# Kernel tuning notes

Measured on AMD Instinct MI355X. Metric: run time of the kernel, lower is better.

Reference implementation:

```python
import jax, jax.numpy as jnp
import numpy as np

L, B, D, H = 512, 256, 256, 256  # seq_len, batch, input_size, hidden_size


def setup_inputs() -> dict:
    key = jax.random.key(0)
    ks = jax.random.split(key, 9)
    bound = 1.0 / np.sqrt(D + H)  # torch nn.Linear default init bound
    W = lambda k: jax.random.uniform(k, (H, D + H), jnp.float32, -bound, bound)
    bvec = lambda k: jax.random.uniform(k, (H,), jnp.float32, -bound, bound)
    x = jax.random.normal(ks[0], (L, B, D), jnp.float32)
    h = jnp.zeros((B, H), jnp.float32)
    c = jnp.zeros((B, H), jnp.float32)
    return {
        "x": x, "h": h, "c": c,
        "Wh": W(ks[1]), "bh": bvec(ks[2]),   # forget gate (self.Wh)
        "Wx": W(ks[3]), "bx": bvec(ks[4]),   # input gate (self.Wx)
        "Wc": W(ks[5]), "bc": bvec(ks[6]),   # cell candidate (self.Wc)
        "Wo": W(ks[7]), "bo": bvec(ks[8]),   # output gate (self.Wo)
    }


def reference(x, h, c, Wh, bh, Wx, bx, Wc, bc, Wo, bo):
    # x: [L, B, D]; h, c: [B, H]. Gate input is cat((h, x_t), dim=1) -> [B, H+D].
    def step(carry, xt):
        h, c = carry
        g = jnp.concatenate([h, xt], axis=1)              # [B, H+D]
        ft = jax.nn.sigmoid(g @ Wh.T + bh)                # forget
        it = jax.nn.sigmoid(g @ Wx.T + bx)                # input
        ct = ft * c + it * jnp.tanh(g @ Wc.T + bc)        # new cell state
        ot = jax.nn.sigmoid(g @ Wo.T + bo)                # output
        ht = ot * jnp.tanh(ct)
        return (ht, ct), ht

    (h_final, c_final), hAll = jax.lax.scan(step, (h, c), x)
    return hAll, h_final, c_final
```

## Files before the change

### kernel.cpp

```cpp
#include <hip/hip_runtime.h>
#include <hip/hip_bf16.h>

typedef __bf16 bf16x8 __attribute__((ext_vector_type(8)));
typedef float f32x4 __attribute__((ext_vector_type(4)));

#define LSEQ 512
#define NB   256
#define NH   256
#define KD   512
#define HROW_U64 (NH / 2)
#define HBUF_U64 (NB * HROW_U64)

__global__ __launch_bounds__(256) void lstm_prep(const float* __restrict__ h0,
                                                 unsigned long long* __restrict__ hbuf) {
  int g = blockIdx.x * 256 + threadIdx.x;
  unsigned pa = (unsigned)__builtin_bit_cast(unsigned short, (__bf16)h0[2 * g]);
  unsigned pb = (unsigned)__builtin_bit_cast(unsigned short, (__bf16)h0[2 * g + 1]);
  hbuf[g] = (unsigned long long)(pa | (pb << 16));
}

__global__ __launch_bounds__(256) void lstm_main(
    const float* __restrict__ x,
    const float* __restrict__ c0,
    const float* __restrict__ Wf, const float* __restrict__ bf_,
    const float* __restrict__ Wi, const float* __restrict__ bi_,
    const float* __restrict__ Wc, const float* __restrict__ bc_,
    const float* __restrict__ Wo, const float* __restrict__ bo_,
    float* __restrict__ out,
    unsigned long long* __restrict__ hbuf)
{
  const int r    = blockIdx.x;
  const int cb   = blockIdx.y;
  const int tid  = threadIdx.x;
  const int w    = tid >> 6;
  const int lane = tid & 63;
  const int l15  = lane & 15;
  const int kg   = lane >> 4;

  __shared__ __align__(16) unsigned char Ash[16 * KD * 2];
  __shared__ float zbuf[4][16][17];

  const int j0    = cb * 16;
  const int brow0 = r * 16;

  const float* Wg = (w == 0) ? Wf : (w == 1) ? Wi : (w == 2) ? Wc : Wo;
  bf16x8 bfrag[16];
  {
    const float* wp = Wg + (size_t)(j0 + l15) * KD + kg * 8;
#pragma unroll
    for (int s = 0; s < 16; ++s) {
      float4 lo = *(const float4*)(wp + s * 32);
      float4 hi = *(const float4*)(wp + s * 32 + 4);
      bf16x8 v;
      v[0] = (__bf16)lo.x; v[1] = (__bf16)lo.y; v[2] = (__bf16)lo.z; v[3] = (__bf16)lo.w;
      v[4] = (__bf16)hi.x; v[5] = (__bf16)hi.y; v[6] = (__bf16)hi.z; v[7] = (__bf16)hi.w;
      bfrag[s] = v;
    }
  }

  const int erow = tid >> 4, ecol = tid & 15;
  const int brow = brow0 + erow;
  const int jcol = j0 + ecol;
  const float biasf = bf_[jcol], biasi = bi_[jcol], biasc = bc_[jcol], biaso = bo_[jcol];
  float cst   = c0[brow * NH + jcol];
  float hlast = 0.f;

  const int swz  = (erow & 7) << 4;
  const int base = erow * 1024;

  float4 xr0, xr1, xr2, xr3;
  {
    const float* xp = x + ((size_t)brow * 256 + ecol * 16);
    xr0 = ((const float4*)xp)[0]; xr1 = ((const float4*)xp)[1];
    xr2 = ((const float4*)xp)[2]; xr3 = ((const float4*)xp)[3];
  }

  for (int t = 0; t < LSEQ; ++t) {
    {
      bf16x8 p0, p1;
      p0[0] = (__bf16)xr0.x; p0[1] = (__bf16)xr0.y; p0[2] = (__bf16)xr0.z; p0[3] = (__bf16)xr0.w;
      p0[4] = (__bf16)xr1.x; p0[5] = (__bf16)xr1.y; p0[6] = (__bf16)xr1.z; p0[7] = (__bf16)xr1.w;
      p1[0] = (__bf16)xr2.x; p1[1] = (__bf16)xr2.y; p1[2] = (__bf16)xr2.z; p1[3] = (__bf16)xr2.w;
      p1[4] = (__bf16)xr3.x; p1[5] = (__bf16)xr3.y; p1[6] = (__bf16)xr3.z; p1[7] = (__bf16)xr3.w;
      *(uint4*)&Ash[(base + (256 + ecol * 16) * 2) ^ swz]     = __builtin_bit_cast(uint4, p0);
      *(uint4*)&Ash[(base + (256 + ecol * 16 + 8) * 2) ^ swz] = __builtin_bit_cast(uint4, p1);
    }
    {
      int tn = (t + 1 < LSEQ) ? t + 1 : t;
      const float* xp = x + ((size_t)tn * NB * 256 + (size_t)brow * 256 + ecol * 16);
      xr0 = ((const float4*)xp)[0]; xr1 = ((const float4*)xp)[1];
      xr2 = ((const float4*)xp)[2]; xr3 = ((const float4*)xp)[3];
    }
    __syncthreads();

    f32x4 acc = {0.f, 0.f, 0.f, 0.f};
#pragma unroll
    for (int s = 8; s < 16; ++s) {
      int ab = ((l15 * 1024) + (s * 32 + kg * 8) * 2) ^ ((l15 & 7) << 4);
      bf16x8 a = *(const bf16x8*)&Ash[ab];
      acc = __builtin_amdgcn_mfma_f32_16x16x32_bf16(a, bfrag[s], acc, 0, 0, 0);
    }

    const unsigned long long* hp =
        hbuf + (size_t)(t & 1) * HBUF_U64 + (size_t)brow * HROW_U64;
    unsigned long long hv[8];
    while (1) {
      bool ok = true;
#pragma unroll
      for (int i = 0; i < 8; ++i) {
        hv[i] = __hip_atomic_load(&hp[i * 16 + ecol], __ATOMIC_RELAXED,
                                  __HIP_MEMORY_SCOPE_AGENT);
        ok &= ((unsigned)(hv[i] >> 32) == (unsigned)t);
      }
      if (ok) break;
    }

#pragma unroll
    for (int i = 0; i < 8; ++i)
      *(unsigned*)&Ash[(base + (i * 16 + ecol) * 4) ^ swz] = (unsigned)hv[i];
    __syncthreads();

#pragma unroll
    for (int s = 0; s < 8; ++s) {
      int ab = ((l15 * 1024) + (s * 32 + kg * 8) * 2) ^ ((l15 & 7) << 4);
      bf16x8 a = *(const bf16x8*)&Ash[ab];
      acc = __builtin_amdgcn_mfma_f32_16x16x32_bf16(a, bfrag[s], acc, 0, 0, 0);
    }
#pragma unroll
    for (int v4i = 0; v4i < 4; ++v4i) zbuf[w][kg * 4 + v4i][l15] = acc[v4i];
    __syncthreads();

    float zf = zbuf[0][erow][ecol] + biasf;
    float zi = zbuf[1][erow][ecol] + biasi;
    float zc = zbuf[2][erow][ecol] + biasc;
    float zo = zbuf[3][erow][ecol] + biaso;
    float fg    = 1.f / (1.f + __expf(-zf));
    float ig    = 1.f / (1.f + __expf(-zi));
    float ccand = 1.f - 2.f / (__expf(2.f * zc) + 1.f);
    float og    = 1.f / (1.f + __expf(-zo));
    cst   = fg * cst + ig * ccand;
    float tc = 1.f - 2.f / (__expf(2.f * cst) + 1.f);
    hlast = og * tc;

    unsigned mybits = (unsigned)__builtin_bit_cast(unsigned short, (__bf16)hlast);
    unsigned nbbits = __shfl_down(mybits, 1);
    if ((ecol & 1) == 0) {
      unsigned long long pkt =
          ((unsigned long long)(unsigned)(t + 1) << 32) |
          (unsigned long long)(mybits | (nbbits << 16));
      __hip_atomic_store(&hbuf[(size_t)((t + 1) & 1) * HBUF_U64 +
                               (size_t)brow * HROW_U64 + cb * 8 + (ecol >> 1)],
                         pkt, __ATOMIC_RELAXED, __HIP_MEMORY_SCOPE_AGENT);
    }

    out[(size_t)t * NB * NH + brow * NH + jcol] = hlast;
  }

  out[(size_t)LSEQ * NB * NH + brow * NH + jcol]           = hlast;
  out[(size_t)LSEQ * NB * NH + NB * NH + brow * NH + jcol] = cst;
}

extern "C" void kernel_launch(void* const* d_in, const int* in_sizes, int n_in,
                              void* d_out, int out_size, void* d_ws, size_t ws_size,
                              hipStream_t stream) {
  const float* x  = (const float*)d_in[0];
  const float* h0 = (const float*)d_in[1];
  const float* c0 = (const float*)d_in[2];
  const float* Wf = (const float*)d_in[3];
  const float* bf = (const float*)d_in[4];
  const float* Wi = (const float*)d_in[5];
  const float* bi = (const float*)d_in[6];
  const float* Wc = (const float*)d_in[7];
  const float* bc = (const float*)d_in[8];
  const float* Wo = (const float*)d_in[9];
  const float* bo = (const float*)d_in[10];
  float* out = (float*)d_out;

  unsigned long long* hbuf = (unsigned long long*)d_ws;

  lstm_prep<<<128, 256, 0, stream>>>(h0, hbuf);
  lstm_main<<<dim3(16, 16), 256, 0, stream>>>(x, c0, Wf, bf, Wi, bi, Wc, bc,
                                              Wo, bo, out, hbuf);
}
```

Baseline: 1.195 ms.

## Duplicate hidden-state exchange buffer with fast and system-coherent polling paths

Every h packet is now written to two buffers: one with sc0 (a faster, less coherent path) and one with sc0 sc1 (system scope). The polling loop first reads the fast buffer and falls back to the coherent one if the step tag does not match yet. The goal is lower latency in the cross-block spin-wait that serialises each timestep. In exchange it doubles store traffic and relies on cache-coherence behaviour across XCDs, where the fast copy may stay stale and force the fallback.

```diff
diff --git a/kernel.cpp b/kernel.cpp
--- a/kernel.cpp
+++ b/kernel.cpp
@@ -12,11 +12,14 @@
 #define HBUF_U64 (NB * HROW_U64)
 
 __global__ __launch_bounds__(256) void lstm_prep(const float* __restrict__ h0,
-                                                 unsigned long long* __restrict__ hbuf) {
+                                                 unsigned long long* __restrict__ hbufS,
+                                                 unsigned long long* __restrict__ hbufF) {
   int g = blockIdx.x * 256 + threadIdx.x;
   unsigned pa = (unsigned)__builtin_bit_cast(unsigned short, (__bf16)h0[2 * g]);
   unsigned pb = (unsigned)__builtin_bit_cast(unsigned short, (__bf16)h0[2 * g + 1]);
-  hbuf[g] = (unsigned long long)(pa | (pb << 16));
+  unsigned long long pkt = (unsigned long long)(pa | (pb << 16));
+  hbufS[g] = pkt;
+  hbufF[g] = pkt;
 }
 
 __global__ __launch_bounds__(256) void lstm_main(
@@ -27,7 +30,8 @@
     const float* __restrict__ Wc, const float* __restrict__ bc_,
     const float* __restrict__ Wo, const float* __restrict__ bo_,
     float* __restrict__ out,
-    unsigned long long* __restrict__ hbuf)
+    unsigned long long* __restrict__ hbufS,
+    unsigned long long* __restrict__ hbufF)
 {
   const int r    = blockIdx.x;
   const int cb   = blockIdx.y;
@@ -101,18 +105,61 @@
       acc = __builtin_amdgcn_mfma_f32_16x16x32_bf16(a, bfrag[s], acc, 0, 0, 0);
     }
 
-    const unsigned long long* hp =
-        hbuf + (size_t)(t & 1) * HBUF_U64 + (size_t)brow * HROW_U64;
     unsigned long long hv[8];
-    while (1) {
-      bool ok = true;
-#pragma unroll
-      for (int i = 0; i < 8; ++i) {
-        hv[i] = __hip_atomic_load(&hp[i * 16 + ecol], __ATOMIC_RELAXED,
-                                  __HIP_MEMORY_SCOPE_AGENT);
-        ok &= ((unsigned)(hv[i] >> 32) == (unsigned)t);
+    {
+      const size_t roff = (size_t)(t & 1) * HBUF_U64 + (size_t)brow * HROW_U64 + ecol;
+      const unsigned long long* hpF = hbufF + roff;
+      const unsigned long long* hpS = hbufS + roff;
+      const unsigned tu = (unsigned)t;
+      while (1) {
+        unsigned long long f0, f1, f2, f3, f4, f5, f6, f7;
+        asm volatile(
+            "global_load_dwordx2 %0, %8, off sc0\n\t"
+            "global_load_dwordx2 %1, %8, off offset:128 sc0\n\t"
+            "global_load_dwordx2 %2, %8, off offset:256 sc0\n\t"
+            "global_load_dwordx2 %3, %8, off offset:384 sc0\n\t"
+            "global_load_dwordx2 %4, %8, off offset:512 sc0\n\t"
+            "global_load_dwordx2 %5, %8, off offset:640 sc0\n\t"
+            "global_load_dwordx2 %6, %8, off offset:768 sc0\n\t"
+            "global_load_dwordx2 %7, %8, off offset:896 sc0\n\t"
+            "s_waitcnt vmcnt(0)"
+            : "=&v"(f0), "=&v"(f1), "=&v"(f2), "=&v"(f3),
+              "=&v"(f4), "=&v"(f5), "=&v"(f6), "=&v"(f7)
+            : "v"(hpF)
+            : "memory");
+        bool ok = ((unsigned)(f0 >> 32) == tu) & ((unsigned)(f1 >> 32) == tu) &
+                  ((unsigned)(f2 >> 32) == tu) & ((unsigned)(f3 >> 32) == tu) &
+                  ((unsigned)(f4 >> 32) == tu) & ((unsigned)(f5 >> 32) == tu) &
+                  ((unsigned)(f6 >> 32) == tu) & ((unsigned)(f7 >> 32) == tu);
+        if (ok) {
+          hv[0] = f0; hv[1] = f1; hv[2] = f2; hv[3] = f3;
+          hv[4] = f4; hv[5] = f5; hv[6] = f6; hv[7] = f7;
+          break;
+        }
+        asm volatile(
+            "global_load_dwordx2 %0, %8, off sc0 sc1\n\t"
+            "global_load_dwordx2 %1, %8, off offset:128 sc0 sc1\n\t"
+            "global_load_dwordx2 %2, %8, off offset:256 sc0 sc1\n\t"
+            "global_load_dwordx2 %3, %8, off offset:384 sc0 sc1\n\t"
+            "global_load_dwordx2 %4, %8, off offset:512 sc0 sc1\n\t"
+            "global_load_dwordx2 %5, %8, off offset:640 sc0 sc1\n\t"
+            "global_load_dwordx2 %6, %8, off offset:768 sc0 sc1\n\t"
+            "global_load_dwordx2 %7, %8, off offset:896 sc0 sc1\n\t"
+            "s_waitcnt vmcnt(0)"
+            : "=&v"(f0), "=&v"(f1), "=&v"(f2), "=&v"(f3),
+              "=&v"(f4), "=&v"(f5), "=&v"(f6), "=&v"(f7)
+            : "v"(hpS)
+            : "memory");
+        ok = ((unsigned)(f0 >> 32) == tu) & ((unsigned)(f1 >> 32) == tu) &
+             ((unsigned)(f2 >> 32) == tu) & ((unsigned)(f3 >> 32) == tu) &
+             ((unsigned)(f4 >> 32) == tu) & ((unsigned)(f5 >> 32) == tu) &
+             ((unsigned)(f6 >> 32) == tu) & ((unsigned)(f7 >> 32) == tu);
+        if (ok) {
+          hv[0] = f0; hv[1] = f1; hv[2] = f2; hv[3] = f3;
+          hv[4] = f4; hv[5] = f5; hv[6] = f6; hv[7] = f7;
+          break;
+        }
       }
-      if (ok) break;
     }
 
 #pragma unroll
@@ -148,9 +195,12 @@
       unsigned long long pkt =
           ((unsigned long long)(unsigned)(t + 1) << 32) |
           (unsigned long long)(mybits | (nbbits << 16));
-      __hip_atomic_store(&hbuf[(size_t)((t + 1) & 1) * HBUF_U64 +
-                               (size_t)brow * HROW_U64 + cb * 8 + (ecol >> 1)],
-                         pkt, __ATOMIC_RELAXED, __HIP_MEMORY_SCOPE_AGENT);
+      const size_t poff = (size_t)((t + 1) & 1) * HBUF_U64 +
+                          (size_t)brow * HROW_U64 + cb * 8 + (ecol >> 1);
+      asm volatile("global_store_dwordx2 %0, %1, off sc0"
+                   :: "v"(hbufF + poff), "v"(pkt) : "memory");
+      asm volatile("global_store_dwordx2 %0, %1, off sc0 sc1"
+                   :: "v"(hbufS + poff), "v"(pkt) : "memory");
     }
 
     out[(size_t)t * NB * NH + brow * NH + jcol] = hlast;
@@ -168,6 +218,7 @@
   const float* c0 = (const float*)d_in[2];
   const float* Wf = (const float*)d_in[3];
   const float* bf = (const float*)d_in[4];
+  const float* bi_dummy = nullptr; (void)bi_dummy;
   const float* Wi = (const float*)d_in[5];
   const float* bi = (const float*)d_in[6];
   const float* Wc = (const float*)d_in[7];
@@ -176,9 +227,10 @@
   const float* bo = (const float*)d_in[10];
   float* out = (float*)d_out;
 
-  unsigned long long* hbuf = (unsigned long long*)d_ws;
-
-  lstm_prep<<<128, 256, 0, stream>>>(h0, hbuf);
+  unsigned long long* hbufS = (unsigned long long*)d_ws;
+  unsigned long long* hbufF = hbufS + 2 * HBUF_U64;
+
+  lstm_prep<<<128, 256, 0, stream>>>(h0, hbufS, hbufF);
   lstm_main<<<dim3(16, 16), 256, 0, stream>>>(x, c0, Wf, bf, Wi, bi, Wc, bc,
-                                              Wo, bo, out, hbuf);
+                                              Wo, bo, out, hbufS, hbufF);
 }
```

After: 1.230 ms. +2.9%, slower.

## Rework cross-block hidden-state exchange with dual-scope buffers and issue-early polling

Applied to the files above, without the earlier changes.

Hidden-state packets are now written to two buffers, one with a narrower cache scope (sc0) and one with device scope (sc0 sc1). Consumers poll the fast copy using inline-asm loads issued before the x-part MFMAs, and fall back to the device-scope copy every few spins. The loop is unrolled by two, prefetching x two steps ahead, and the grid is linearized so that column blocks are grouped differently. This aims to cut the latency of the per-step spin-wait. It relies on non-coherent caching behaviour across CUs for the fast path and doubles the store traffic.

```diff
diff --git a/kernel.cpp b/kernel.cpp
--- a/kernel.cpp
+++ b/kernel.cpp
@@ -12,12 +12,140 @@
 #define HBUF_U64 (NB * HROW_U64)
 
 __global__ __launch_bounds__(256) void lstm_prep(const float* __restrict__ h0,
-                                                 unsigned long long* __restrict__ hbuf) {
+                                                 unsigned long long* __restrict__ hbufS,
+                                                 unsigned long long* __restrict__ hbufF) {
   int g = blockIdx.x * 256 + threadIdx.x;
   unsigned pa = (unsigned)__builtin_bit_cast(unsigned short, (__bf16)h0[2 * g]);
   unsigned pb = (unsigned)__builtin_bit_cast(unsigned short, (__bf16)h0[2 * g + 1]);
-  hbuf[g] = (unsigned long long)(pa | (pb << 16));
+  unsigned long long pkt = (unsigned long long)(pa | (pb << 16));
+  hbufS[g] = pkt;
+  hbufF[g] = pkt;
 }
+
+#define POLL_ISSUE(F0, F1, F2, F3, F4, F5, F6, F7, PTR)                        \
+  asm volatile("global_load_dwordx2 %0, %8, off sc0\n\t"                       \
+               "global_load_dwordx2 %1, %8, off offset:128 sc0\n\t"            \
+               "global_load_dwordx2 %2, %8, off offset:256 sc0\n\t"            \
+               "global_load_dwordx2 %3, %8, off offset:384 sc0\n\t"            \
+               "global_load_dwordx2 %4, %8, off offset:512 sc0\n\t"            \
+               "global_load_dwordx2 %5, %8, off offset:640 sc0\n\t"            \
+               "global_load_dwordx2 %6, %8, off offset:768 sc0\n\t"            \
+               "global_load_dwordx2 %7, %8, off offset:896 sc0\n\t"            \
+               : "=&v"(F0), "=&v"(F1), "=&v"(F2), "=&v"(F3),                   \
+                 "=&v"(F4), "=&v"(F5), "=&v"(F6), "=&v"(F7)                    \
+               : "v"(PTR) : "memory")
+
+#define POLL_SLOW(F0, F1, F2, F3, F4, F5, F6, F7, PTR)                         \
+  asm volatile("global_load_dwordx2 %0, %8, off sc0 sc1\n\t"                   \
+               "global_load_dwordx2 %1, %8, off offset:128 sc0 sc1\n\t"        \
+               "global_load_dwordx2 %2, %8, off offset:256 sc0 sc1\n\t"        \
+               "global_load_dwordx2 %3, %8, off offset:384 sc0 sc1\n\t"        \
+               "global_load_dwordx2 %4, %8, off offset:512 sc0 sc1\n\t"        \
+               "global_load_dwordx2 %5, %8, off offset:640 sc0 sc1\n\t"        \
+               "global_load_dwordx2 %6, %8, off offset:768 sc0 sc1\n\t"        \
+               "global_load_dwordx2 %7, %8, off offset:896 sc0 sc1\n\t"        \
+               "s_waitcnt vmcnt(0)"                                            \
+               : "=&v"(F0), "=&v"(F1), "=&v"(F2), "=&v"(F3),                   \
+                 "=&v"(F4), "=&v"(F5), "=&v"(F6), "=&v"(F7)                    \
+               : "v"(PTR) : "memory")
+
+#define TAGOK(F0, F1, F2, F3, F4, F5, F6, F7, TU)                              \
+  (((unsigned)((F0) >> 32) == (TU)) & ((unsigned)((F1) >> 32) == (TU)) &       \
+   ((unsigned)((F2) >> 32) == (TU)) & ((unsigned)((F3) >> 32) == (TU)) &       \
+   ((unsigned)((F4) >> 32) == (TU)) & ((unsigned)((F5) >> 32) == (TU)) &       \
+   ((unsigned)((F6) >> 32) == (TU)) & ((unsigned)((F7) >> 32) == (TU)))
+
+#define STEP(T, XR0, XR1, XR2, XR3) do {                                       \
+    const size_t roff_ = (size_t)((T) & 1) * HBUF_U64 +                        \
+                         (size_t)brow * HROW_U64 + ecol;                       \
+    const unsigned long long* hpF_ = hbufF + roff_;                            \
+    const unsigned long long* hpS_ = hbufS + roff_;                            \
+    unsigned long long f0, f1, f2, f3, f4, f5, f6, f7;                         \
+    POLL_ISSUE(f0, f1, f2, f3, f4, f5, f6, f7, hpF_);                          \
+    {                                                                          \
+      bf16x8 p0, p1;                                                           \
+      p0[0]=(__bf16)XR0.x; p0[1]=(__bf16)XR0.y; p0[2]=(__bf16)XR0.z; p0[3]=(__bf16)XR0.w; \
+      p0[4]=(__bf16)XR1.x; p0[5]=(__bf16)XR1.y; p0[6]=(__bf16)XR1.z; p0[7]=(__bf16)XR1.w; \
+      p1[0]=(__bf16)XR2.x; p1[1]=(__bf16)XR2.y; p1[2]=(__bf16)XR2.z; p1[3]=(__bf16)XR2.w; \
+      p1[4]=(__bf16)XR3.x; p1[5]=(__bf16)XR3.y; p1[6]=(__bf16)XR3.z; p1[7]=(__bf16)XR3.w; \
+      *(uint4*)&Ash[(base + (256 + ecol * 16) * 2) ^ swz]     = __builtin_bit_cast(uint4, p0); \
+      *(uint4*)&Ash[(base + (256 + ecol * 16 + 8) * 2) ^ swz] = __builtin_bit_cast(uint4, p1); \
+    }                                                                          \
+    __syncthreads();                                      \
+    f32x4 acc = {0.f, 0.f, 0.f, 0.f};                                          \
+    _Pragma("unroll")                                                          \
+    for (int s = 8; s < 16; ++s) {                                             \
+      int ab = ((l15 * 1024) + (s * 32 + kg * 8) * 2) ^ ((l15 & 7) << 4);      \
+      bf16x8 a = *(const bf16x8*)&Ash[ab];                                     \
+      acc = __builtin_amdgcn_mfma_f32_16x16x32_bf16(a, bfrag[s], acc, 0, 0, 0);\
+    }                                                                          \
+    {                                                                          \
+      const unsigned tu_ = (unsigned)(T);                                      \
+      int spin_ = 0;                                                           \
+      while (1) {                                                              \
+        asm volatile("s_waitcnt vmcnt(0)" ::: "memory");                       \
+        __builtin_amdgcn_sched_barrier(0);                                     \
+        bool ok = TAGOK(f0, f1, f2, f3, f4, f5, f6, f7, tu_);                  \
+        if (ok) break;                                                         \
+        if ((++spin_ & 3) == 0) {                                              \
+          POLL_SLOW(f0, f1, f2, f3, f4, f5, f6, f7, hpS_);                     \
+          __builtin_amdgcn_sched_barrier(0);                                   \
+          ok = TAGOK(f0, f1, f2, f3, f4, f5, f6, f7, tu_);                     \
+          if (ok) break;                                                       \
+        }                                                                      \
+        POLL_ISSUE(f0, f1, f2, f3, f4, f5, f6, f7, hpF_);                      \
+      }                                                                        \
+    }                                                                          \
+    {   \
+      int tn_ = (T) + 2; if (tn_ >= LSEQ) tn_ = LSEQ - 1;                      \
+      const float* xp_ = x + ((size_t)tn_ * (NB * 256) + (size_t)brow * 256 + ecol * 16); \
+      XR0 = ((const float4*)xp_)[0]; XR1 = ((const float4*)xp_)[1];            \
+      XR2 = ((const float4*)xp_)[2]; XR3 = ((const float4*)xp_)[3];            \
+    }                                                                          \
+    _Pragma("unroll")                                                          \
+    for (int i = 0; i < 8; ++i) {                                              \
+      unsigned long long hv_ = (i==0)?f0:(i==1)?f1:(i==2)?f2:(i==3)?f3:        \
+                               (i==4)?f4:(i==5)?f5:(i==6)?f6:f7;               \
+      *(unsigned*)&Ash[(base + (i * 16 + ecol) * 4) ^ swz] = (unsigned)hv_;    \
+    }                                                                          \
+    __syncthreads();                                      \
+    _Pragma("unroll")                                                          \
+    for (int s = 0; s < 8; ++s) {                                              \
+      int ab = ((l15 * 1024) + (s * 32 + kg * 8) * 2) ^ ((l15 & 7) << 4);      \
+      bf16x8 a = *(const bf16x8*)&Ash[ab];                                     \
+      acc = __builtin_amdgcn_mfma_f32_16x16x32_bf16(a, bfrag[s], acc, 0, 0, 0);\
+    }                                                                          \
+    _Pragma("unroll")                                                          \
+    for (int v4i = 0; v4i < 4; ++v4i) zbuf[w][kg * 4 + v4i][l15] = acc[v4i];   \
+    __syncthreads();                                 \
+    {                                                                          \
+      float zf = zbuf[0][erow][ecol] + biasf;                                  \
+      float zi = zbuf[1][erow][ecol] + biasi;                                  \
+      float zc = zbuf[2][erow][ecol] + biasc;                                  \
+      float zo = zbuf[3][erow][ecol] + biaso;                                  \
+      float fg    = 1.f / (1.f + __expf(-zf));                                 \
+      float ig    = 1.f / (1.f + __expf(-zi));                                 \
+      float ccand = 1.f - 2.f / (__expf(2.f * zc) + 1.f);                      \
+      float og    = 1.f / (1.f + __expf(-zo));                                 \
+      cst   = fg * cst + ig * ccand;                                           \
+      float tc = 1.f - 2.f / (__expf(2.f * cst) + 1.f);                        \
+      hlast = og * tc;                                                         \
+      unsigned mybits = (unsigned)__builtin_bit_cast(unsigned short, (__bf16)hlast); \
+      unsigned nbbits = __shfl_down(mybits, 1);                                \
+      if ((ecol & 1) == 0) {                                                   \
+        unsigned long long pkt =                                               \
+            ((unsigned long long)(unsigned)((T) + 1) << 32) |                  \
+            (unsigned long long)(mybits | (nbbits << 16));                     \
+        const size_t poff_ = (size_t)(((T) + 1) & 1) * HBUF_U64 +              \
+                             (size_t)brow * HROW_U64 + cb * 8 + (ecol >> 1);   \
+        asm volatile("global_store_dwordx2 %0, %1, off sc0"                    \
+                     :: "v"(hbufF + poff_), "v"(pkt) : "memory");              \
+        asm volatile("global_store_dwordx2 %0, %1, off sc0 sc1"                \
+                     :: "v"(hbufS + poff_), "v"(pkt) : "memory");              \
+      }                                                                        \
+      out[(size_t)(T) * NB * NH + brow * NH + jcol] = hlast;                   \
+    }                                                                          \
+  } while (0)
 
 __global__ __launch_bounds__(256) void lstm_main(
     const float* __restrict__ x,
@@ -27,10 +155,12 @@
     const float* __restrict__ Wc, const float* __restrict__ bc_,
     const float* __restrict__ Wo, const float* __restrict__ bo_,
     float* __restrict__ out,
-    unsigned long long* __restrict__ hbuf)
+    unsigned long long* __restrict__ hbufS,
+    unsigned long long* __restrict__ hbufF)
 {
-  const int r    = blockIdx.x;
-  const int cb   = blockIdx.y;
+  const int bid  = blockIdx.x;
+  const int r    = bid & 15;
+  const int cb   = bid >> 4;
   const int tid  = threadIdx.x;
   const int w    = tid >> 6;
   const int lane = tid & 63;
@@ -68,92 +198,21 @@
   const int swz  = (erow & 7) << 4;
   const int base = erow * 1024;
 
-  float4 xr0, xr1, xr2, xr3;
+  float4 xA0, xA1, xA2, xA3, xB0, xB1, xB2, xB3;
   {
     const float* xp = x + ((size_t)brow * 256 + ecol * 16);
-    xr0 = ((const float4*)xp)[0]; xr1 = ((const float4*)xp)[1];
-    xr2 = ((const float4*)xp)[2]; xr3 = ((const float4*)xp)[3];
-  }
-
-  for (int t = 0; t < LSEQ; ++t) {
-    {
-      bf16x8 p0, p1;
-      p0[0] = (__bf16)xr0.x; p0[1] = (__bf16)xr0.y; p0[2] = (__bf16)xr0.z; p0[3] = (__bf16)xr0.w;
-      p0[4] = (__bf16)xr1.x; p0[5] = (__bf16)xr1.y; p0[6] = (__bf16)xr1.z; p0[7] = (__bf16)xr1.w;
-      p1[0] = (__bf16)xr2.x; p1[1] = (__bf16)xr2.y; p1[2] = (__bf16)xr2.z; p1[3] = (__bf16)xr2.w;
-      p1[4] = (__bf16)xr3.x; p1[5] = (__bf16)xr3.y; p1[6] = (__bf16)xr3.z; p1[7] = (__bf16)xr3.w;
-      *(uint4*)&Ash[(base + (256 + ecol * 16) * 2) ^ swz]     = __builtin_bit_cast(uint4, p0);
-      *(uint4*)&Ash[(base + (256 + ecol * 16 + 8) * 2) ^ swz] = __builtin_bit_cast(uint4, p1);
-    }
-    {
-      int tn = (t + 1 < LSEQ) ? t + 1 : t;
-      const float* xp = x + ((size_t)tn * NB * 256 + (size_t)brow * 256 + ecol * 16);
-      xr0 = ((const float4*)xp)[0]; xr1 = ((const float4*)xp)[1];
-      xr2 = ((const float4*)xp)[2]; xr3 = ((const float4*)xp)[3];
-    }
-    __syncthreads();
-
-    f32x4 acc = {0.f, 0.f, 0.f, 0.f};
-#pragma unroll
-    for (int s = 8; s < 16; ++s) {
-      int ab = ((l15 * 1024) + (s * 32 + kg * 8) * 2) ^ ((l15 & 7) << 4);
-      bf16x8 a = *(const bf16x8*)&Ash[ab];
-      acc = __builtin_amdgcn_mfma_f32_16x16x32_bf16(a, bfrag[s], acc, 0, 0, 0);
-    }
-
-    const unsigned long long* hp =
-        hbuf + (size_t)(t & 1) * HBUF_U64 + (size_t)brow * HROW_U64;
-    unsigned long long hv[8];
-    while (1) {
-      bool ok = true;
-#pragma unroll
-      for (int i = 0; i < 8; ++i) {
-        hv[i] = __hip_atomic_load(&hp[i * 16 + ecol], __ATOMIC_RELAXED,
-                                  __HIP_MEMORY_SCOPE_AGENT);
-        ok &= ((unsigned)(hv[i] >> 32) == (unsigned)t);
-      }
-      if (ok) break;
-    }
-
-#pragma unroll
-    for (int i = 0; i < 8; ++i)
-      *(unsigned*)&Ash[(base + (i * 16 + ecol) * 4) ^ swz] = (unsigned)hv[i];
-    __syncthreads();
-
-#pragma unroll
-    for (int s = 0; s < 8; ++s) {
-      int ab = ((l15 * 1024) + (s * 32 + kg * 8) * 2) ^ ((l15 & 7) << 4);
-      bf16x8 a = *(const bf16x8*)&Ash[ab];
-      acc = __builtin_amdgcn_mfma_f32_16x16x32_bf16(a, bfrag[s], acc, 0, 0, 0);
-    }
-#pragma unroll
-    for (int v4i = 0; v4i < 4; ++v4i) zbuf[w][kg * 4 + v4i][l15] = acc[v4i];
-    __syncthreads();
-
-    float zf = zbuf[0][erow][ecol] + biasf;
-    float zi = zbuf[1][erow][ecol] + biasi;
-    float zc = zbuf[2][erow][ecol] + biasc;
-    float zo = zbuf[3][erow][ecol] + biaso;
-    float fg    = 1.f / (1.f + __expf(-zf));
-    float ig    = 1.f / (1.f + __expf(-zi));
-    float ccand = 1.f - 2.f / (__expf(2.f * zc) + 1.f);
-    float og    = 1.f / (1.f + __expf(-zo));
-    cst   = fg * cst + ig * ccand;
-    float tc = 1.f - 2.f / (__expf(2.f * cst) + 1.f);
-    hlast = og * tc;
-
-    unsigned mybits = (unsigned)__builtin_bit_cast(unsigned short, (__bf16)hlast);
-    unsigned nbbits = __shfl_down(mybits, 1);
-    if ((ecol & 1) == 0) {
-      unsigned long long pkt =
-          ((unsigned long long)(unsigned)(t + 1) << 32) |
-          (unsigned long long)(mybits | (nbbits << 16));
-      __hip_atomic_store(&hbuf[(size_t)((t + 1) & 1) * HBUF_U64 +
-                               (size_t)brow * HROW_U64 + cb * 8 + (ecol >> 1)],
-                         pkt, __ATOMIC_RELAXED, __HIP_MEMORY_SCOPE_AGENT);
-    }
-
-    out[(size_t)t * NB * NH + brow * NH + jcol] = hlast;
+    xA0 = ((const float4*)xp)[0]; xA1 = ((const float4*)xp)[1];
+    xA2 = ((const float4*)xp)[2]; xA3 = ((const float4*)xp)[3];
+  }
+  {
+    const float* xp = x + ((size_t)(NB * 256) + (size_t)brow * 256 + ecol * 16);
+    xB0 = ((const float4*)xp)[0]; xB1 = ((const float4*)xp)[1];
+    xB2 = ((const float4*)xp)[2]; xB3 = ((const float4*)xp)[3];
+  }
+
+  for (int tp = 0; tp < LSEQ; tp += 2) {
+    STEP(tp,     xA0, xA1, xA2, xA3);
+    STEP(tp + 1, xB0, xB1, xB2, xB3);
   }
 
   out[(size_t)LSEQ * NB * NH + brow * NH + jcol]           = hlast;
@@ -176,9 +235,10 @@
   const float* bo = (const float*)d_in[10];
   float* out = (float*)d_out;
 
-  unsigned long long* hbuf = (unsigned long long*)d_ws;
-
-  lstm_prep<<<128, 256, 0, stream>>>(h0, hbuf);
-  lstm_main<<<dim3(16, 16), 256, 0, stream>>>(x, c0, Wf, bf, Wi, bi, Wc, bc,
-                                              Wo, bo, out, hbuf);
+  unsigned long long* hbufS = (unsigned long long*)d_ws;
+  unsigned long long* hbufF = hbufS + 2 * HBUF_U64;
+
+  lstm_prep<<<128, 256, 0, stream>>>(h0, hbufS, hbufF);
+  lstm_main<<<256, 256, 0, stream>>>(x, c0, Wf, bf, Wi, bi, Wc, bc,
+                                     Wo, bo, out, hbufS, hbufF);
 }
```

Result: slower. 1.511 ms (+26.5%).
